# Kernel optimization log

Measured on AMD Instinct MI355X. Metric: run time of the kernel, lower is better.

The kernel has to match this reference:

```python
import jax, jax.numpy as jnp
import numpy as np

B, C, U, LEN, K = 32, 16, 16, 128, 4  # batch, channels, units, image side, cheb order
POWERS = K + 1


def _path_chebyshev(n, k):
    """Chebyshev polynomials T_0..T_k of the rescaled normalized Laplacian of an
    undirected path graph with n nodes. Returns [k+1, n, n] float32."""
    A = np.zeros((n, n), dtype=np.float64)
    A[np.arange(n - 1), np.arange(1, n)] = 1.0
    A = A + A.T
    d = A.sum(axis=1)
    dinv = 1.0 / np.sqrt(d)
    L = np.eye(n) - dinv[:, None] * A * dinv[None, :]   # normalized Laplacian
    Lt = L - np.eye(n)                                   # rescaled: 2L/lambda_max - I, lambda_max=2
    T = [np.eye(n), Lt]
    for _ in range(2, k + 1):
        T.append(2.0 * Lt @ T[-1] - T[-2])
    return np.stack(T[: k + 1]).astype(np.float32)


def setup_inputs() -> dict:
    key = jax.random.key(0)
    kx, kc = jax.random.split(key)
    x = jax.random.normal(kx, (B, C, LEN, LEN), dtype=jnp.float32)
    coefs = 0.001 * jax.random.normal(kc, (POWERS, POWERS, C, U), dtype=jnp.float32)
    cheb = jnp.asarray(_path_chebyshev(LEN, K))  # same graph for both axes
    return {"x": x, "coefs": coefs, "cheb1": cheb, "cheb2": cheb}


def reference(x, coefs, cheb1, cheb2):
    # out[b,u,p,q] = sum_{k1,k2,c,h,w} coefs[k1,k2,c,u] * cheb1[k1,h,p] * x[b,c,h,w] * cheb2[k2,w,q]
    t1 = jnp.einsum('bchw,khp->bkcpw', x, cheb1)        # apply cheb1 along H
    s = jnp.einsum('bkcpw,klcu->blupw', t1, coefs)      # contract k1 and channels
    out = jnp.einsum('blupw,lwq->bupq', s, cheb2)       # apply cheb2 along W, contract k2
    return out
```

## Files before the change

kernel.cpp:

```cpp
#include <hip/hip_runtime.h>
#include <hip/hip_bf16.h>

#define LEN 128
#define NB 32
#define NC 16
#define NU 16
#define NK 5
#define KC 80
#define KCP 96

typedef unsigned int uint32;
typedef unsigned short ushort16;
typedef __attribute__((ext_vector_type(8))) short bf16x8;
typedef __attribute__((ext_vector_type(4))) float f32x4;

#define MFMA(a, b, c) __builtin_amdgcn_mfma_f32_16x16x32_bf16(a, b, c, 0, 0, 0)

#define SIG(r) (((r) & 15) ^ (((r) >> 3) & 15))

static __device__ inline ushort16 f2bf(float f) {
    union { float f; uint32 u; } v; v.f = f;
    uint32 u = v.u;
    uint32 r = (u + 0x7fffu + ((u >> 16) & 1u)) >> 16;
    return (ushort16)r;
}
static __device__ inline uint32 pkbf(float a, float b) {
    return (uint32)f2bf(a) | ((uint32)f2bf(b) << 16);
}
static __device__ inline bf16x8 frag16(const void* p) {
    return *(const bf16x8*)p;
}

__global__ __launch_bounds__(256) void kprep(const float* __restrict__ x,
                                             const float* __restrict__ coefs,
                                             const float* __restrict__ cheb1,
                                             const float* __restrict__ cheb2,
                                             ushort16* __restrict__ xF,
                                             ushort16* __restrict__ cheb1F,
                                             ushort16* __restrict__ cheb2F,
                                             ushort16* __restrict__ coefF) {
    __shared__ __align__(16) uint32 Xs[128 * 64];
    const int blk = blockIdx.x, tid = threadIdx.x;
    if (blk < 512) {
        const int bc = blk;
        const float* xp = x + (size_t)bc * (LEN * LEN);
        {
            int w = tid & 127, hg = tid >> 7;
            #pragma unroll
            for (int uu = 0; uu < 8; ++uu) {
                int u = hg * 8 + uu;
                uint4 d;
                uint32* dp = (uint32*)&d;
                #pragma unroll
                for (int t = 0; t < 4; ++t) {
                    int h2 = u * 4 + t;
                    dp[t] = pkbf(xp[(2 * h2) * LEN + w], xp[(2 * h2 + 1) * LEN + w]);
                }
                *(uint4*)(Xs + w * 64 + ((u ^ SIG(w)) << 2)) = d;
            }
        }
        __syncthreads();
        ushort16* dst = xF + (size_t)bc * 16384;
        #pragma unroll
        for (int i = 0; i < 8; ++i) {
            int n = tid + i * 256;
            int lane = n & 63, fk = n >> 6;
            int wrow = (fk >> 2) * 16 + (lane & 15);
            int u = (fk & 3) * 4 + (lane >> 4);
            uint4 v = *(const uint4*)(Xs + wrow * 64 + ((u ^ SIG(wrow)) << 2));
            *(uint4*)(dst + (size_t)n * 8) = v;
        }
    } else {
        int i = (blk - 512) * 256 + tid;
        if (i < 81920) {
            int j = i & 7, lane = (i >> 3) & 63, ks = (i >> 9) & 3, nt = i >> 11;
            int kp = nt * 16 + (lane & 15);
            int k = kp >> 7, p = kp & 127;
            int h = ks * 32 + ((lane >> 4) << 3) + j;
            cheb1F[i] = f2bf(cheb1[(k * LEN + h) * LEN + p]);
        } else if (i < 163840) {
            int i2 = i - 81920;
            int j = i2 & 7, lane = (i2 >> 3) & 63, t = i2 >> 9;
            int ks = t % 20, nt = t / 20;
            int q = nt * 16 + (lane & 15);
            int lw = ks * 32 + ((lane >> 4) << 3) + j;
            int l = lw >> 7, w = lw & 127;
            cheb2F[i2] = f2bf(cheb2[(l * LEN + w) * LEN + q]);
        } else {
            int i3 = i - 163840;
            int j = i3 & 7, lane = (i3 >> 3) & 63, t = i3 >> 9;
            int ks = t % 3, nt = t / 3;
            int lu = nt * 16 + (lane & 15);
            int l = lu >> 4, u = lu & 15;
            int kc = ks * 32 + ((lane >> 4) << 3) + j;
            int k = kc >> 4, c = kc & 15;
            coefF[i3] = (kc < KC) ? f2bf(coefs[((k * NK + l) * NC + c) * NU + u]) : (ushort16)0;
        }
    }
}

__global__ __launch_bounds__(256, 5) void k1_mfma(const ushort16* __restrict__ xF,
                                                  const ushort16* __restrict__ cheb1F,
                                                  ushort16* __restrict__ t1, int b0) {
    __shared__ __align__(16) uint32 Bs[80 * 64];
    const int c = blockIdx.x, bl = blockIdx.y, ns = blockIdx.z;
    const int b = b0 + bl;
    const int tid = threadIdx.x;
    const int lane = tid & 63, wm = tid >> 6;
    const int m16 = lane & 15, g = lane >> 4;

    const ushort16* xFb = xF + ((size_t)(b * NC + c)) * 16384;

    f32x4 acc[2][5];
    #pragma unroll
    for (int mi = 0; mi < 2; ++mi)
        #pragma unroll
        for (int ni = 0; ni < 5; ++ni) acc[mi][ni] = (f32x4)0.f;

    #pragma unroll
    for (int ks = 0; ks < 4; ++ks) {
        bf16x8 Af[2], Bf[5];
        #pragma unroll
        for (int mi = 0; mi < 2; ++mi) {
            int mt = wm * 2 + mi;
            Af[mi] = frag16(xFb + ((size_t)(mt * 4 + ks) * 64 + lane) * 8);
        }
        #pragma unroll
        for (int ni = 0; ni < 5; ++ni) {
            int nt = ns * 5 + ni;
            Bf[ni] = frag16(cheb1F + ((size_t)(nt * 4 + ks) * 64 + lane) * 8);
        }
        #pragma unroll
        for (int mi = 0; mi < 2; ++mi)
            #pragma unroll
            for (int ni = 0; ni < 5; ++ni)
                acc[mi][ni] = MFMA(Af[mi], Bf[ni], acc[mi][ni]);
    }

    #pragma unroll
    for (int ni = 0; ni < 5; ++ni)
        #pragma unroll
        for (int mi = 0; mi < 2; ++mi) {
            int rr = ni * 16 + m16;
            int wu = wm * 32 + mi * 16 + g * 4;
            uint2 d;
            d.x = pkbf(acc[mi][ni][0], acc[mi][ni][1]);
            d.y = pkbf(acc[mi][ni][2], acc[mi][ni][3]);
            int u = wu >> 3;
            *(uint2*)(Bs + rr * 64 + ((u ^ SIG(rr)) << 2) + ((wu >> 1) & 3)) = d;
        }
    __syncthreads();

    #pragma unroll
    for (int i = 0; i < 5; ++i) {
        int n = tid + i * 256;
        int rr = n >> 4, wsg = n & 15;
        uint4 v = *(const uint4*)(Bs + rr * 64 + ((wsg ^ SIG(rr)) << 2));
        int kp = ns * 80 + rr;
        int k = kp >> 7, p = kp & 127;
        *(uint4*)(t1 + ((size_t)((bl * LEN + p) * KC + k * NC + c)) * LEN + wsg * 8) = v;
    }
}

__global__ __launch_bounds__(256, 5) void k2_mfma(const ushort16* __restrict__ t1,
                                                  const ushort16* __restrict__ coefF,
                                                  const ushort16* __restrict__ cheb2F,
                                                  float* __restrict__ out, int b0) {
    __shared__ __align__(16) uint32 sm[128 * 64];
    const int p = blockIdx.x, bl = blockIdx.y, b = b0 + bl;
    const int tid = threadIdx.x;
    const int lane = tid & 63, wave = tid >> 6;
    const int n16 = lane & 15, g = lane >> 4;

    const uint32* t1u = (const uint32*)(t1 + (size_t)(bl * LEN + p) * (KC * LEN));
    uint4 Av[3], Bv[3];
    #pragma unroll
    for (int i = 0; i < 3; ++i) {
        int it = tid + i * 256;
        if (it < 640) {
            int a2 = it >> 4, wq = it & 15;
            const uint32* src = t1u + a2 * 128 + wq * 4;
            Av[i] = *(const uint4*)(src);
            Bv[i] = *(const uint4*)(src + 64);
        }
    }
    #pragma unroll
    for (int i = 0; i < 4; ++i) {
        int idx = tid + i * 256;
        int row = idx >> 3, d = idx & 7;
        int u = 10 + (d >> 2);
        sm[row * 64 + ((u ^ SIG(row)) << 2) + (d & 3)] = 0;
    }
    #pragma unroll
    for (int i = 0; i < 3; ++i) {
        int it = tid + i * 256;
        if (it < 640) {
            int a2 = it >> 4, wq = it & 15;
            const uint32* av = (const uint32*)&Av[i];
            const uint32* bv = (const uint32*)&Bv[i];
            int u = a2 >> 2, lo = a2 & 3;
            #pragma unroll
            for (int j = 0; j < 4; ++j) {
                int r0 = wq * 8 + 2 * j, r1 = r0 + 1;
                sm[r0 * 64 + ((u ^ SIG(r0)) << 2) + lo] = (av[j] & 0xffffu) | (bv[j] << 16);
                sm[r1 * 64 + ((u ^ SIG(r1)) << 2) + lo] = (av[j] >> 16) | (bv[j] & 0xffff0000u);
            }
        }
    }
    __syncthreads();

    f32x4 acc[2][5];
    #pragma unroll
    for (int mi = 0; mi < 2; ++mi)
        #pragma unroll
        for (int ni = 0; ni < 5; ++ni) acc[mi][ni] = (f32x4)0.f;

    #pragma unroll
    for (int ks = 0; ks < 3; ++ks) {
        bf16x8 Af[2], Bf[5];
        #pragma unroll
        for (int mi = 0; mi < 2; ++mi) {
            int row = wave * 32 + mi * 16 + n16;
            Af[mi] = frag16(sm + row * 64 + (((ks * 4 + g) ^ SIG(row)) << 2));
        }
        #pragma unroll
        for (int ni = 0; ni < 5; ++ni)
            Bf[ni] = frag16(coefF + ((size_t)(ni * 3 + ks) * 64 + lane) * 8);
        #pragma unroll
        for (int mi = 0; mi < 2; ++mi)
            #pragma unroll
            for (int ni = 0; ni < 5; ++ni)
                acc[mi][ni] = MFMA(Af[mi], Bf[ni], acc[mi][ni]);
    }
    __syncthreads();

    {
        ushort16* A3 = (ushort16*)sm;
        #pragma unroll
        for (int mi = 0; mi < 2; ++mi)
            #pragma unroll
            for (int ni = 0; ni < 5; ++ni) {
                int wcol = wave * 32 + mi * 16 + g * 4;
                uint2 d;
                d.x = pkbf(acc[mi][ni][0], acc[mi][ni][1]);
                d.y = pkbf(acc[mi][ni][2], acc[mi][ni][3]);
                *(uint2*)(A3 + n16 * 648 + ni * 128 + wcol) = d;
            }
    }
    __syncthreads();

    const ushort16* A3r = (const ushort16*)sm;
    f32x4 c3[2];
    c3[0] = (f32x4)0.f; c3[1] = (f32x4)0.f;
    #pragma unroll 4
    for (int ks = 4; ks < 20; ++ks) {
        bf16x8 Aa = frag16(A3r + n16 * 648 + ks * 32 + g * 8);
        #pragma unroll
        for (int nt = 0; nt < 2; ++nt) {
            bf16x8 Bb = frag16(cheb2F + ((size_t)((wave * 2 + nt) * 20 + ks) * 64 + lane) * 8);
            c3[nt] = MFMA(Aa, Bb, c3[nt]);
        }
    }

    #pragma unroll
    for (int nt = 0; nt < 2; ++nt)
        #pragma unroll
        for (int r = 0; r < 4; ++r) {
            int u = g * 4 + r;
            int q = wave * 32 + nt * 16 + n16;
            uint32 bf = ((uint32)A3r[u * 648 + q]) << 16;
            float l0 = __uint_as_float(bf);
            out[(((size_t)(b * NU + u)) * LEN + p) * LEN + q] = c3[nt][r] + l0;
        }
}

extern "C" void kernel_launch(void* const* d_in, const int* in_sizes, int n_in,
                              void* d_out, int out_size, void* d_ws, size_t ws_size,
                              hipStream_t stream) {
    const float* x     = (const float*)d_in[0];
    const float* coefs = (const float*)d_in[1];
    const float* cheb1 = (const float*)d_in[2];
    const float* cheb2 = (const float*)d_in[3];
    float* out = (float*)d_out;

    const size_t xF_bytes  = (size_t)NB * NC * 16384 * sizeof(ushort16);
    const size_t aux_bytes = 163840 + 163840 + 15360;
    size_t off = (ws_size - aux_bytes - xF_bytes) & ~(size_t)255;
    ushort16* cheb1F = (ushort16*)((char*)d_ws + off);
    ushort16* cheb2F = cheb1F + 81920;
    ushort16* coefF  = cheb2F + 81920;
    ushort16* xF     = coefF + 7680;
    ushort16* t1 = (ushort16*)d_ws;

    const size_t per_b = (size_t)LEN * KC * LEN * sizeof(ushort16);
    int chunk = (int)(off / per_b);
    if (chunk < 1) chunk = 1;
    if (chunk > NB) chunk = NB;

    hipLaunchKernelGGL(kprep, dim3(1182), dim3(256), 0, stream,
                       x, coefs, cheb1, cheb2, xF, cheb1F, cheb2F, coefF);
    for (int b0 = 0; b0 < NB; b0 += chunk) {
        int cb = (NB - b0 < chunk) ? (NB - b0) : chunk;
        hipLaunchKernelGGL(k1_mfma, dim3(NC, cb, 8), dim3(256), 0, stream,
                           xF, cheb1F, t1, b0);
        hipLaunchKernelGGL(k2_mfma, dim3(LEN, cb), dim3(256), 0, stream,
                           t1, coefF, cheb2F, out, b0);
    }
}
```

Before: 146.9 us.

## Skip identity Chebyshev term in k1 and stage cheb1 fragments in LDS

The first Chebyshev polynomial T0 is the identity, so its slice of t1 is now written by converting x straight to bf16 in the z==0 blocks. The MFMA work in k1 covers only k=1..4, cutting its matrix work by a fifth. The cheb1 B-fragments for each block are loaded once into swizzled LDS, and the wave tiling changes to 4x2 with 64 rows per block. The z==0 blocks carry the extra copy work, which creates some load imbalance, and occupancy drops to 4 blocks per CU because of the added LDS.

```diff
diff --git a/kernel.cpp b/kernel.cpp
--- a/kernel.cpp
+++ b/kernel.cpp
@@ -99,50 +99,79 @@
     }
 }
 
-__global__ __launch_bounds__(256, 5) void k1_mfma(const ushort16* __restrict__ xF,
+__global__ __launch_bounds__(256, 4) void k1_mfma(const ushort16* __restrict__ xF,
                                                   const ushort16* __restrict__ cheb1F,
+                                                  const float* __restrict__ x,
                                                   ushort16* __restrict__ t1, int b0) {
-    __shared__ __align__(16) uint32 Bs[80 * 64];
-    const int c = blockIdx.x, bl = blockIdx.y, ns = blockIdx.z;
+    __shared__ __align__(16) uint32 Ls[64 * 64];
+    __shared__ __align__(16) uint32 Bs[64 * 64];
+    const int c = blockIdx.x, bl = blockIdx.y, z = blockIdx.z;
     const int b = b0 + bl;
     const int tid = threadIdx.x;
-    const int lane = tid & 63, wm = tid >> 6;
+    const int lane = tid & 63, wave = tid >> 6;
     const int m16 = lane & 15, g = lane >> 4;
+    const int wm = wave >> 1, wn = wave & 1;
+
+    #pragma unroll
+    for (int i = 0; i < 4; ++i) {
+        int u = tid + i * 256;
+        int ln = u & 63, ks = (u >> 6) & 3, nt = u >> 8;
+        uint4 v = *(const uint4*)(cheb1F + ((size_t)(((8 + z * 4 + nt) * 4 + ks) * 64 + ln)) * 8);
+        int row = nt * 16 + (ln & 15), hu = ks * 4 + (ln >> 4);
+        *(uint4*)(Ls + row * 64 + ((hu ^ SIG(row)) << 2)) = v;
+    }
+
+    if (z == 0) {
+        const float* xp = x + (size_t)(b * NC + c) * (LEN * LEN);
+        int p = tid >> 1, half = tid & 1;
+        const float4* src = (const float4*)(xp + p * LEN + half * 64);
+        ushort16* dst = t1 + ((size_t)(bl * LEN + p) * KC + c) * LEN + half * 64;
+        #pragma unroll
+        for (int i = 0; i < 16; ++i) {
+            float4 v = src[i];
+            uint2 d;
+            d.x = pkbf(v.x, v.y);
+            d.y = pkbf(v.z, v.w);
+            *(uint2*)(dst + i * 4) = d;
+        }
+    }
+    __syncthreads();
 
     const ushort16* xFb = xF + ((size_t)(b * NC + c)) * 16384;
 
-    f32x4 acc[2][5];
-    #pragma unroll
-    for (int mi = 0; mi < 2; ++mi)
-        #pragma unroll
-        for (int ni = 0; ni < 5; ++ni) acc[mi][ni] = (f32x4)0.f;
+    f32x4 acc[4][2];
+    #pragma unroll
+    for (int mi = 0; mi < 4; ++mi)
+        #pragma unroll
+        for (int ni = 0; ni < 2; ++ni) acc[mi][ni] = (f32x4)0.f;
 
     #pragma unroll
     for (int ks = 0; ks < 4; ++ks) {
-        bf16x8 Af[2], Bf[5];
-        #pragma unroll
-        for (int mi = 0; mi < 2; ++mi) {
-            int mt = wm * 2 + mi;
+        bf16x8 Af[4], Bf[2];
+        #pragma unroll
+        for (int mi = 0; mi < 4; ++mi) {
+            int mt = wm * 4 + mi;
             Af[mi] = frag16(xFb + ((size_t)(mt * 4 + ks) * 64 + lane) * 8);
         }
         #pragma unroll
-        for (int ni = 0; ni < 5; ++ni) {
-            int nt = ns * 5 + ni;
-            Bf[ni] = frag16(cheb1F + ((size_t)(nt * 4 + ks) * 64 + lane) * 8);
-        }
-        #pragma unroll
-        for (int mi = 0; mi < 2; ++mi)
-            #pragma unroll
-            for (int ni = 0; ni < 5; ++ni)
+        for (int ni = 0; ni < 2; ++ni) {
+            int row = (wn * 2 + ni) * 16 + m16;
+            int hu = ks * 4 + g;
+            Bf[ni] = frag16(Ls + row * 64 + ((hu ^ SIG(row)) << 2));
+        }
+        #pragma unroll
+        for (int mi = 0; mi < 4; ++mi)
+            #pragma unroll
+            for (int ni = 0; ni < 2; ++ni)
                 acc[mi][ni] = MFMA(Af[mi], Bf[ni], acc[mi][ni]);
     }
 
     #pragma unroll
-    for (int ni = 0; ni < 5; ++ni)
-        #pragma unroll
-        for (int mi = 0; mi < 2; ++mi) {
-            int rr = ni * 16 + m16;
-            int wu = wm * 32 + mi * 16 + g * 4;
+    for (int ni = 0; ni < 2; ++ni)
+        #pragma unroll
+        for (int mi = 0; mi < 4; ++mi) {
+            int rr = (wn * 2 + ni) * 16 + m16;
+            int wu = (wm * 4 + mi) * 16 + g * 4;
             uint2 d;
             d.x = pkbf(acc[mi][ni][0], acc[mi][ni][1]);
             d.y = pkbf(acc[mi][ni][2], acc[mi][ni][3]);
@@ -152,11 +181,11 @@
     __syncthreads();
 
     #pragma unroll
-    for (int i = 0; i < 5; ++i) {
+    for (int i = 0; i < 4; ++i) {
         int n = tid + i * 256;
         int rr = n >> 4, wsg = n & 15;
         uint4 v = *(const uint4*)(Bs + rr * 64 + ((wsg ^ SIG(rr)) << 2));
-        int kp = ns * 80 + rr;
+        int kp = 128 + z * 64 + rr;
         int k = kp >> 7, p = kp & 127;
         *(uint4*)(t1 + ((size_t)((bl * LEN + p) * KC + k * NC + c)) * LEN + wsg * 8) = v;
     }
@@ -302,7 +331,7 @@
     for (int b0 = 0; b0 < NB; b0 += chunk) {
         int cb = (NB - b0 < chunk) ? (NB - b0) : chunk;
         hipLaunchKernelGGL(k1_mfma, dim3(NC, cb, 8), dim3(256), 0, stream,
-                           xF, cheb1F, t1, b0);
+                           xF, cheb1F, x, t1, b0);
         hipLaunchKernelGGL(k2_mfma, dim3(LEN, cb), dim3(256), 0, stream,
                            t1, coefF, cheb2F, out, b0);
     }
```

New measurement: 152.6 us. +3.9%, slower.
